# Kernel optimization log

Measured on AMD Instinct MI355X. Metric: run time of the kernel, lower is better.

## Reference

```python
import jax, jax.numpy as jnp
import numpy as np


def gru_cell(x, h, Wih, Whh, bih, bhh):
    # torch GRU cell, gate order r, z, n
    gi = x @ Wih.T + bih
    gh = h @ Whh.T + bhh
    ir, iz, inn = jnp.split(gi, 3, axis=-1)
    hr, hz, hn = jnp.split(gh, 3, axis=-1)
    r = jax.nn.sigmoid(ir + hr)
    z = jax.nn.sigmoid(iz + hz)
    n = jnp.tanh(inn + r * hn)
    return (1.0 - z) * n + z * h


def setup_inputs() -> dict:
    key = jax.random.key(0)
    ks = jax.random.split(key, 24)
    S, T, B, E, H, V = 64, 64, 32, 512, 1024, 32000
    sc_e = 1.0 / np.sqrt(E)
    sc_h = 1.0 / np.sqrt(H)

    def rn(i, shape, sc):
        return jax.random.normal(ks[i], shape, jnp.float32) * sc

    return {
        "src": jax.random.randint(ks[0], (S, B), 0, V),
        "trg": jax.random.randint(ks[1], (T, B), 0, V),
        "emb": rn(2, (V, E), 0.02),
        # encoder forward-direction GRU
        "Wih_f": rn(3, (3 * H, E), sc_e), "Whh_f": rn(4, (3 * H, H), sc_h),
        "bih_f": rn(5, (3 * H,), sc_h), "bhh_f": rn(6, (3 * H,), sc_h),
        # encoder backward-direction GRU
        "Wih_b": rn(7, (3 * H, E), sc_e), "Whh_b": rn(8, (3 * H, H), sc_h),
        "bih_b": rn(9, (3 * H,), sc_h), "bhh_b": rn(10, (3 * H,), sc_h),
        # attention: Linear(2H -> H) and scoring vector v
        "Wa": rn(11, (H, 2 * H), sc_h), "ba": rn(12, (H,), sc_h),
        "v": rn(13, (H,), sc_h),
        # decoder GRU: input is [embedded(E); context(H)]
        "Wih_d": rn(14, (3 * H, E + H), sc_h), "Whh_d": rn(15, (3 * H, H), sc_h),
        "bih_d": rn(16, (3 * H,), sc_h), "bhh_d": rn(17, (3 * H,), sc_h),
        # output head Linear(2H -> V)
        "Wout": rn(18, (V, 2 * H), sc_h), "bout": rn(19, (V,), sc_h),
    }


def reference(src, trg, emb, Wih_f, Whh_f, bih_f, bhh_f, Wih_b, Whh_b, bih_b, bhh_b,
              Wa, ba, v, Wih_d, Whh_d, bih_d, bhh_d, Wout, bout):
    S, B = src.shape
    H = Whh_f.shape[1]

    # ---- encoder: bidirectional GRU, fwd+bwd output halves summed ----
    src_emb = emb[src]  # [S, B, E]
    h0 = jnp.zeros((B, H), src_emb.dtype)

    def step_f(h, x):
        h2 = gru_cell(x, h, Wih_f, Whh_f, bih_f, bhh_f)
        return h2, h2

    def step_b(h, x):
        h2 = gru_cell(x, h, Wih_b, Whh_b, bih_b, bhh_b)
        return h2, h2

    h_fwd, out_f = jax.lax.scan(step_f, h0, src_emb)
    _, out_b_rev = jax.lax.scan(step_b, h0, src_emb[::-1])
    enc_out = out_f + out_b_rev[::-1]          # [S, B, H]
    enc_bt = enc_out.transpose(1, 0, 2)        # [B, S, H]

    # ---- decoder with teacher forcing (ratio fixed to 1.0) ----
    dec_tokens = jnp.concatenate([src[-1:], trg[:-1]], axis=0)  # [T, B]
    dec_emb = emb[dec_tokens]                                   # [T, B, E]

    def dec_step(h, e_t):
        # Bahdanau attention: relu(Linear([h; enc])) scored by v
        hrep = jnp.broadcast_to(h[:, None, :], enc_bt.shape)    # [B, S, H]
        energy = jax.nn.relu(jnp.concatenate([hrep, enc_bt], -1) @ Wa.T + ba)
        scores = energy @ v                                     # [B, S]
        a = jax.nn.softmax(scores, axis=1)
        ctx = jnp.einsum('bs,bsh->bh', a, enc_bt)               # [B, H]
        rnn_in = jnp.concatenate([e_t, ctx], axis=-1)           # [B, E+H]
        h_new = gru_cell(rnn_in, h, Wih_d, Whh_d, bih_d, bhh_d)
        logits = jnp.concatenate([h_new, ctx], -1) @ Wout.T + bout  # [B, V]
        return h_new, logits

    _, outputs = jax.lax.scan(dec_step, h_fwd, dec_emb)  # [T, B, V]
    return outputs
```

## Files before the change

kernel.cpp:

```cpp
#include <hip/hip_runtime.h>
#include <hip/hip_bf16.h>

#define S_ 64
#define T_ 64
#define B_ 32
#define E_ 512
#define H_ 1024
#define V_ 32000
#define H3 3072
#define H2 2048
#define EH 1536

typedef unsigned short u16;
typedef unsigned int u32;
typedef unsigned long long u64;
typedef __attribute__((ext_vector_type(8))) short bf16x8;
typedef __attribute__((ext_vector_type(4))) float f32x4;

#define MFMA3(ACC, AH_, AL_, BH_, BL_)                                              \
    ACC = __builtin_amdgcn_mfma_f32_16x16x32_bf16(AL_, BH_, ACC, 0, 0, 0);          \
    ACC = __builtin_amdgcn_mfma_f32_16x16x32_bf16(AH_, BL_, ACC, 0, 0, 0);          \
    ACC = __builtin_amdgcn_mfma_f32_16x16x32_bf16(AH_, BH_, ACC, 0, 0, 0);

__device__ __forceinline__ void splitf(float x, u16& h, u16& l) {
    u32 xb = __float_as_uint(x);
    u32 hb = (xb + 0x7FFFu + ((xb >> 16) & 1u)) & 0xFFFF0000u;
    h = (u16)(hb >> 16);
    float lf = x - __uint_as_float(hb);
    u32 lb = __float_as_uint(lf);
    l = (u16)((lb + 0x7FFFu + ((lb >> 16) & 1u)) >> 16);
}

__device__ __forceinline__ float bf2f(u16 v) { return __uint_as_float(((u32)v) << 16); }

__device__ __forceinline__ void load_lds16(const void* g, void* l) {
    __builtin_amdgcn_global_load_lds((const __attribute__((address_space(1))) u32*)g,
                                     (__attribute__((address_space(3))) u32*)l, 16, 0, 0);
}

__device__ __forceinline__ bf16x8 ld_sys16(const u16* p) {
    union { bf16x8 v; u64 q[2]; } u;
    const u64* q = (const u64*)p;
    u.q[0] = __hip_atomic_load(q,     __ATOMIC_RELAXED, __HIP_MEMORY_SCOPE_SYSTEM);
    u.q[1] = __hip_atomic_load(q + 1, __ATOMIC_RELAXED, __HIP_MEMORY_SCOPE_SYSTEM);
    return u.v;
}
__device__ __forceinline__ float ld_sysf(const float* p) {
    return __hip_atomic_load(p, __ATOMIC_RELAXED, __HIP_MEMORY_SCOPE_SYSTEM);
}
__device__ __forceinline__ void st_sysf(float* p, float v) {
    __hip_atomic_store(p, v, __ATOMIC_RELAXED, __HIP_MEMORY_SCOPE_SYSTEM);
}
__device__ __forceinline__ void st_sysu16(u16* p, u16 v) {
    __hip_atomic_store(p, v, __ATOMIC_RELAXED, __HIP_MEMORY_SCOPE_SYSTEM);
}

__device__ __forceinline__ void gbar(int* cnt, int* flag, int nblk, int blk, int& gen) {
    __syncthreads();
    if (threadIdx.x == 0) {
        gen += 1;
        asm volatile("s_waitcnt vmcnt(0)" ::: "memory");
        __hip_atomic_fetch_add(&cnt[(blk & 7) << 5], 1, __ATOMIC_RELAXED,
                               __HIP_MEMORY_SCOPE_SYSTEM);
        if (blk == 0) {
            const int target = nblk * gen;
            for (;;) {
                int sum = 0;
#pragma unroll
                for (int j = 0; j < 8; ++j)
                    sum += __hip_atomic_load(&cnt[j << 5], __ATOMIC_RELAXED,
                                             __HIP_MEMORY_SCOPE_SYSTEM);
                if (sum >= target) break;
                __builtin_amdgcn_s_sleep(2);
            }
#pragma unroll
            for (int j = 0; j < 8; ++j)
                __hip_atomic_store(&flag[j << 5], gen, __ATOMIC_RELAXED,
                                   __HIP_MEMORY_SCOPE_SYSTEM);
        } else {
            while (__hip_atomic_load(&flag[(blk & 7) << 5], __ATOMIC_RELAXED,
                                     __HIP_MEMORY_SCOPE_SYSTEM) < gen)
                __builtin_amdgcn_s_sleep(2);
        }
    }
    __syncthreads();
}

__global__ void k_embed_src_split(const int* __restrict__ src, const float* __restrict__ emb,
                                  u16* __restrict__ hi, u16* __restrict__ lo) {
    int row = blockIdx.x;
    int tok = src[row];
    int c = threadIdx.x * 4;
    float4 v = *reinterpret_cast<const float4*>(emb + (size_t)tok * E_ + c);
    ushort4 h, l;
    splitf(v.x, h.x, l.x); splitf(v.y, h.y, l.y);
    splitf(v.z, h.z, l.z); splitf(v.w, h.w, l.w);
    *reinterpret_cast<ushort4*>(hi + (size_t)row * E_ + c) = h;
    *reinterpret_cast<ushort4*>(lo + (size_t)row * E_ + c) = l;
}

__global__ void k_embed_dec_split(const int* __restrict__ src, const int* __restrict__ trg,
                                  const float* __restrict__ emb,
                                  u16* __restrict__ hi, u16* __restrict__ lo) {
    int row = blockIdx.x;
    int t = row >> 5, b = row & 31;
    int tok = (t == 0) ? src[(S_ - 1) * B_ + b] : trg[(t - 1) * B_ + b];
    int c = threadIdx.x * 4;
    float4 v = *reinterpret_cast<const float4*>(emb + (size_t)tok * E_ + c);
    ushort4 h, l;
    splitf(v.x, h.x, l.x); splitf(v.y, h.y, l.y);
    splitf(v.z, h.z, l.z); splitf(v.w, h.w, l.w);
    *reinterpret_cast<ushort4*>(hi + (size_t)row * E_ + c) = h;
    *reinterpret_cast<ushort4*>(lo + (size_t)row * E_ + c) = l;
}

__global__ __launch_bounds__(256) void k_split(const float* __restrict__ in, int ld, int cols4,
                                               u16* __restrict__ hi, u16* __restrict__ lo) {
    int c4 = blockIdx.x * 256 + threadIdx.x;
    if (c4 >= cols4) return;
    size_t r = blockIdx.y;
    float4 v = *reinterpret_cast<const float4*>(in + r * ld + (size_t)c4 * 4);
    ushort4 h, l;
    splitf(v.x, h.x, l.x); splitf(v.y, h.y, l.y);
    splitf(v.z, h.z, l.z); splitf(v.w, h.w, l.w);
    size_t o = (r * cols4 + c4) * 4;
    *reinterpret_cast<ushort4*>(hi + o) = h;
    *reinterpret_cast<ushort4*>(lo + o) = l;
}

__global__ __launch_bounds__(256) void k_split_sum_enc(
    const float* __restrict__ ef, const float* __restrict__ eb, float* __restrict__ es,
    u16* __restrict__ hi, u16* __restrict__ lo) {
    size_t r = blockIdx.y;
    int c4 = threadIdx.x * 4;
    float4 va = *reinterpret_cast<const float4*>(ef + r * H_ + c4);
    float4 vb = *reinterpret_cast<const float4*>(eb + r * H_ + c4);
    float4 v; v.x = va.x + vb.x; v.y = va.y + vb.y; v.z = va.z + vb.z; v.w = va.w + vb.w;
    *reinterpret_cast<float4*>(es + r * H_ + c4) = v;
    ushort4 h, l;
    splitf(v.x, h.x, l.x); splitf(v.y, h.y, l.y);
    splitf(v.z, h.z, l.z); splitf(v.w, h.w, l.w);
    *reinterpret_cast<ushort4*>(hi + r * H_ + c4) = h;
    *reinterpret_cast<ushort4*>(lo + r * H_ + c4) = l;
}

__global__ void k_wsplit_perm(const float* __restrict__ src, int ld, int coff,
                              u16* __restrict__ hi, u16* __restrict__ lo) {
    int r = blockIdx.x;
    int i = r / 3, g = r - i * 3;
    const float* p = src + (size_t)(g * H_ + i) * ld + coff;
    int c = threadIdx.x * 4;
    float4 v = *reinterpret_cast<const float4*>(p + c);
    ushort4 h, l;
    splitf(v.x, h.x, l.x); splitf(v.y, h.y, l.y);
    splitf(v.z, h.z, l.z); splitf(v.w, h.w, l.w);
    *reinterpret_cast<ushort4*>(hi + (size_t)r * H_ + c) = h;
    *reinterpret_cast<ushort4*>(lo + (size_t)r * H_ + c) = l;
}

__global__ __launch_bounds__(256, 2) void k_gemm_mfma3(
    const u16* __restrict__ Ah, const u16* __restrict__ Al,
    const u16* __restrict__ Bh, const u16* __restrict__ Bl,
    const float* __restrict__ bias, float* __restrict__ C,
    int ldc, int K)
{
    __shared__ u16 ls[4][128 * 32];
    const int tid = threadIdx.x;
    const int lane = tid & 63, w = tid >> 6;
    const int wr = w >> 1, wc = w & 1;
    const size_t m0 = (size_t)blockIdx.x * 128, n0 = (size_t)blockIdx.y * 128;

    const int c0 = (w * 2) * 64 + lane;
    const int r0 = c0 >> 2, kc0 = (c0 & 3) << 3;
    const size_t rstep = (size_t)16 * K;
    const u16* gAh = Ah + (m0 + r0) * K + kc0;
    const u16* gAl = Al + (m0 + r0) * K + kc0;
    const u16* gBh = Bh + (n0 + r0) * K + kc0;
    const u16* gBl = Bl + (n0 + r0) * K + kc0;
    const int lo0 = c0 * 8;

    const int frow = lane & 15, fk = (lane >> 4) << 3;
    const int offA = (wr * 64 + frow) * 32 + fk;
    const int offB = (wc * 64 + frow) * 32 + fk;

    f32x4 acc[4][4] = {};

    for (int k0 = 0; k0 < K; k0 += 32) {
        load_lds16(gAh + k0, &ls[0][lo0]);
        load_lds16(gAh + rstep + k0, &ls[0][lo0 + 512]);
        load_lds16(gAl + k0, &ls[1][lo0]);
        load_lds16(gAl + rstep + k0, &ls[1][lo0 + 512]);
        load_lds16(gBh + k0, &ls[2][lo0]);
        load_lds16(gBh + rstep + k0, &ls[2][lo0 + 512]);
        load_lds16(gBl + k0, &ls[3][lo0]);
        load_lds16(gBl + rstep + k0, &ls[3][lo0 + 512]);
        __syncthreads();

        bf16x8 fAh[4], fAl[4], fBh[4], fBl[4];
#pragma unroll
        for (int m = 0; m < 4; ++m) {
            fAh[m] = *reinterpret_cast<const bf16x8*>(&ls[0][offA + m * 512]);
            fAl[m] = *reinterpret_cast<const bf16x8*>(&ls[1][offA + m * 512]);
        }
#pragma unroll
        for (int n = 0; n < 4; ++n) {
            fBh[n] = *reinterpret_cast<const bf16x8*>(&ls[2][offB + n * 512]);
            fBl[n] = *reinterpret_cast<const bf16x8*>(&ls[3][offB + n * 512]);
        }
#pragma unroll
        for (int m = 0; m < 4; ++m)
#pragma unroll
            for (int n = 0; n < 4; ++n) {
                MFMA3(acc[m][n], fAh[m], fAl[m], fBh[n], fBl[n]);
            }
        __syncthreads();
    }

    const int crow0 = wr * 64 + ((lane >> 4) << 2);
    const int ccol0 = wc * 64 + (lane & 15);
#pragma unroll
    for (int n = 0; n < 4; ++n) {
        const size_t col = n0 + ccol0 + n * 16;
        const float bv = bias ? bias[col] : 0.f;
#pragma unroll
        for (int m = 0; m < 4; ++m)
#pragma unroll
            for (int r = 0; r < 4; ++r)
                C[(m0 + crow0 + m * 16 + r) * (size_t)ldc + col] = acc[m][n][r] + bv;
    }
}

__global__ __launch_bounds__(256, 2) void k_gemm_n2f(
    const u16* __restrict__ Ah, const u16* __restrict__ Al,
    const float* __restrict__ Bf,
    const float* __restrict__ bias, float* __restrict__ C,
    int ldc, int K)
{
    __shared__ u16 lsA[2][128 * 32];
    __shared__ u16 lsBh[256 * 32];
    __shared__ u16 lsBl[256 * 32];
    const int tid = threadIdx.x;
    const int lane = tid & 63, w = tid >> 6;
    const int wr = w >> 1, wc = w & 1;
    const size_t m0 = (size_t)blockIdx.x * 128, n0 = (size_t)blockIdx.y * 256;

    const int frow = lane & 15, fk = (lane >> 4) << 3;
    const int offA = (wr * 64 + frow) * 32 + fk;
    const int offB = (wc * 128 + frow) * 32 + fk;

    f32x4 acc[4][8] = {};

    for (int k0 = 0; k0 < K; k0 += 32) {
#pragma unroll
        for (int q = 0; q < 4; ++q) {
            const int chunk = (w + q * 4) * 64 + lane;
            const int local = chunk & 511;
            const u16* A = (chunk < 512) ? Ah : Al;
            load_lds16(A + (m0 + (local >> 2)) * K + k0 + ((local & 3) << 3),
                       &lsA[chunk >> 9][local * 8]);
        }
#pragma unroll
        for (int q = 0; q < 4; ++q) {
            const int c = tid + q * 256;
            const int row = c >> 2, k8 = (c & 3) << 3;
            const float* src = Bf + (size_t)(n0 + row) * K + k0 + k8;
            float4 v0 = *reinterpret_cast<const float4*>(src);
            float4 v1 = *reinterpret_cast<const float4*>(src + 4);
            union { ushort4 s[2]; bf16x8 v; } hh, ll;
            splitf(v0.x, hh.s[0].x, ll.s[0].x); splitf(v0.y, hh.s[0].y, ll.s[0].y);
            splitf(v0.z, hh.s[0].z, ll.s[0].z); splitf(v0.w, hh.s[0].w, ll.s[0].w);
            splitf(v1.x, hh.s[1].x, ll.s[1].x); splitf(v1.y, hh.s[1].y, ll.s[1].y);
            splitf(v1.z, hh.s[1].z, ll.s[1].z); splitf(v1.w, hh.s[1].w, ll.s[1].w);
            *reinterpret_cast<bf16x8*>(&lsBh[row * 32 + k8]) = hh.v;
            *reinterpret_cast<bf16x8*>(&lsBl[row * 32 + k8]) = ll.v;
        }
        __syncthreads();

        bf16x8 fAh[4], fAl[4];
#pragma unroll
        for (int m = 0; m < 4; ++m) {
            fAh[m] = *reinterpret_cast<const bf16x8*>(&lsA[0][offA + m * 512]);
            fAl[m] = *reinterpret_cast<const bf16x8*>(&lsA[1][offA + m * 512]);
        }
#pragma unroll
        for (int n = 0; n < 8; ++n) {
            bf16x8 fBh = *reinterpret_cast<const bf16x8*>(&lsBh[offB + n * 512]);
            bf16x8 fBl = *reinterpret_cast<const bf16x8*>(&lsBl[offB + n * 512]);
#pragma unroll
            for (int m = 0; m < 4; ++m) {
                MFMA3(acc[m][n], fAh[m], fAl[m], fBh, fBl);
            }
        }
        __syncthreads();
    }

    const int crow0 = wr * 64 + ((lane >> 4) << 2);
    const int ccol0 = wc * 128 + (lane & 15);
#pragma unroll
    for (int n = 0; n < 8; ++n) {
        const size_t col = n0 + ccol0 + n * 16;
        const float bv = bias ? bias[col] : 0.f;
#pragma unroll
        for (int m = 0; m < 4; ++m)
#pragma unroll
            for (int r = 0; r < 4; ++r)
                C[(m0 + crow0 + m * 16 + r) * (size_t)ldc + col] = acc[m][n][r] + bv;
    }
}

__global__ __launch_bounds__(256) void k_enc_persist(
    const u16* __restrict__ whhf_h, const u16* __restrict__ whhf_l,
    const u16* __restrict__ whhb_h, const u16* __restrict__ whhb_l,
    const float* __restrict__ gi_f, const float* __restrict__ gi_b,
    const float* __restrict__ bhh_f, const float* __restrict__ bhh_b,
    u16* __restrict__ hfH0, u16* __restrict__ hfL0,
    u16* __restrict__ hfH1, u16* __restrict__ hfL1,
    u16* __restrict__ hbH0, u16* __restrict__ hbL0,
    u16* __restrict__ hbH1, u16* __restrict__ hbL1,
    float* __restrict__ enc_f, float* __restrict__ enc_b,
    int* __restrict__ cnt, int* __restrict__ flag)
{
    __shared__ __align__(16) char smem[145792];
    u16* lAh  = (u16*)smem;
    u16* lAl  = (u16*)(smem + 65536);
    float* ex0 = (float*)(smem + 131072);
    float* ex1 = (float*)(smem + 137408);
    float* hloc = (float*)(smem + 143744);

    const int blk = blockIdx.x, tid = threadIdx.x;
    const int lane = tid & 63, w = tid >> 6;
    const int dir = blk >> 6, c = blk & 63;
    const int i0 = c * 16;
    const u16* WH = (dir ? whhb_h : whhf_h) + (size_t)c * 48 * 1024;
    const u16* WL = (dir ? whhb_l : whhf_l) + (size_t)c * 48 * 1024;
    const float* gi = dir ? gi_b : gi_f;
    const float* bhh = dir ? bhh_b : bhh_f;
    float* encd = dir ? enc_b : enc_f;
    int gen = 0;

    for (int q = tid; q < 512; q += 256) hloc[q] = 0.f;

    const int frow = lane & 15, fk8 = (lane >> 4) << 3;
    const int cb = lane & 15, rb0 = (lane >> 4) << 2;

    for (int t = 0; t < 64; ++t) {
        const int a = t & 1;
        const u16* rH = dir ? (a ? hbH1 : hbH0) : (a ? hfH1 : hfH0);
        const u16* rL = dir ? (a ? hbL1 : hbL0) : (a ? hfL1 : hfL0);
        u16* oH = dir ? (a ? hbH0 : hbH1) : (a ? hfH0 : hfH1);
        u16* oL = dir ? (a ? hbL0 : hbL1) : (a ? hfL0 : hfL1);
        const int s = dir ? 63 - t : t;

#pragma unroll
        for (int ch0 = 0; ch0 < 4096; ch0 += 256) {
            int ch = ch0 + tid;
            int r = ch >> 7, kc = (ch & 127) << 3;
            int sw = kc ^ ((r & 7) << 3);
            *(bf16x8*)&lAh[r * 1024 + sw] = ld_sys16(&rH[r * 1024 + kc]);
            *(bf16x8*)&lAl[r * 1024 + sw] = ld_sys16(&rL[r * 1024 + kc]);
        }
        __syncthreads();

#pragma unroll
        for (int jj = 0; jj < 3; ++jj) {
            const int j = w * 3 + jj;
            const int m = j & 1;
            const int n = (j >> 1) % 3;
            const int kh = j / 6;
            const int arow = m * 16 + frow;
            const int asw = (arow & 7) << 3;
            const u16* gBh = WH + (size_t)(n * 16 + frow) * 1024;
            const u16* gBl = WL + (size_t)(n * 16 + frow) * 1024;
            f32x4 acc = {};
            const int ke = kh * 512 + 512;
#pragma unroll 4
            for (int k0 = kh * 512; k0 < ke; k0 += 32) {
                int kc = k0 + fk8;
                bf16x8 aH = *(const bf16x8*)&lAh[arow * 1024 + (kc ^ asw)];
                bf16x8 aL = *(const bf16x8*)&lAl[arow * 1024 + (kc ^ asw)];
                bf16x8 bH = *(const bf16x8*)&gBh[kc];
                bf16x8 bL = *(const bf16x8*)&gBl[kc];
                MFMA3(acc, aH, aL, bH, bL);
            }
            float* exd = kh ? ex1 : ex0;
            const int pc = n * 16 + cb;
#pragma unroll
            for (int r = 0; r < 4; ++r)
                exd[pc * 33 + m * 16 + rb0 + r] = acc[r];
        }
        __syncthreads();

        {
            const int il = tid & 15, bb = tid >> 4;
            const int i = i0 + il;
#pragma unroll
            for (int q = 0; q < 2; ++q) {
                int b = bb + q * 16;
                float ghr = ex0[(3 * il + 0) * 33 + b] + ex1[(3 * il + 0) * 33 + b] + bhh[i];
                float ghz = ex0[(3 * il + 1) * 33 + b] + ex1[(3 * il + 1) * 33 + b] + bhh[H_ + i];
                float ghn = ex0[(3 * il + 2) * 33 + b] + ex1[(3 * il + 2) * 33 + b] + bhh[2 * H_ + i];
                size_t gio = (size_t)(s * B_ + b) * H3 + i;
                float gir = gi[gio], giz = gi[gio + H_], gin = gi[gio + 2 * H_];
                float rr = 1.f / (1.f + expf(-(gir + ghr)));
                float zz = 1.f / (1.f + expf(-(giz + ghz)));
                float nn = tanhf(gin + rr * ghn);
                float hold = hloc[b * 16 + il];
                float hnew = (1.f - zz) * nn + zz * hold;
                hloc[b * 16 + il] = hnew;
                u16 hh, hl; splitf(hnew, hh, hl);
                st_sysu16(&oH[b * 1024 + i], hh);
                st_sysu16(&oL[b * 1024 + i], hl);
                encd[((size_t)b * 64 + s) * H_ + i] = hnew;
            }
        }
        gbar(cnt, flag, 128, blk, gen);
    }
}

__global__ __launch_bounds__(256) void k_dec_persist(
    const u16* __restrict__ wah, const u16* __restrict__ wal,
    const u16* __restrict__ wgh, const u16* __restrict__ wgl,
    const u16* __restrict__ wdh, const u16* __restrict__ wdl,
    const float* __restrict__ gi_e, const float* __restrict__ bhh_d,
    const float* __restrict__ ep, const float* __restrict__ vvec,
    const float* __restrict__ enc,
    u16* __restrict__ hH, u16* __restrict__ hL,
    float* __restrict__ hwa, float* __restrict__ scores,
    u16* __restrict__ ctxH, u16* __restrict__ ctxL,
    float* __restrict__ states, int* __restrict__ cnt, int* __restrict__ flag)
{
    __shared__ __align__(16) char smem[140288];
    u16* lWH  = (u16*)smem;
    u16* lWL  = (u16*)(smem + 32768);
    u16* lDH  = (u16*)(smem + 65536);
    float* lenc = (float*)(smem + 98304);
    float* ex1a = (float*)(smem + 131072);
    float* ex1b = (float*)(smem + 133120);
    float* ex2a = (float*)(smem + 135168);
    float* ex2b = (float*)(smem + 137216);
    float* aw   = (float*)(smem + 139264);
    float* hloc = (float*)(smem + 139520);

    const int bid = blockIdx.x, tid = threadIdx.x;
    const int lane = tid & 63, w = tid >> 6;
    const int frow = lane & 15, fk8 = (lane >> 4) << 3;
    const int b3 = bid >> 3, sl = bid & 7;
    int gen = 0;

    for (int ch = tid; ch < 2048; ch += 256) {
        int r = ch >> 7, kc = (ch & 127) << 3;
        int sw = kc ^ ((r & 7) << 3);
        const u16 *sH, *sL;
        if (r < 4) { sH = wah + ((size_t)bid * 4 + r) * 1024;
                     sL = wal + ((size_t)bid * 4 + r) * 1024; }
        else       { sH = wgh + ((size_t)bid * 12 + r - 4) * 1024;
                     sL = wgl + ((size_t)bid * 12 + r - 4) * 1024; }
        *(bf16x8*)&lWH[r * 1024 + sw] = *(const bf16x8*)&sH[kc];
        *(bf16x8*)&lWL[r * 1024 + sw] = *(const bf16x8*)&sL[kc];
    }
    for (int ch = tid; ch < 2048; ch += 256) {
        int r = ch >> 7, kc = (ch & 127) << 3;
        int sw = kc ^ ((r & 7) << 3);
        int rowg = (r < 12) ? bid * 12 + r : bid * 12;
        *(bf16x8*)&lDH[r * 1024 + sw] = *(const bf16x8*)&wdh[(size_t)rowg * 1024 + kc];
    }
    for (int ch = tid; ch < 2048; ch += 256) {
        int s = ch >> 5, c4 = (ch & 31) << 2;
        *(float4*)&lenc[s * 128 + c4] =
            *(const float4*)&enc[((size_t)b3 * 64 + s) * 1024 + sl * 128 + c4];
    }
    if (tid < 128) {
        int b = tid >> 2, u = bid * 4 + (tid & 3);
        hloc[tid] = bf2f(hH[b * 1024 + u]) + bf2f(hL[b * 1024 + u]);
    }
    float vreg[16];
#pragma unroll
    for (int i = 0; i < 16; ++i) vreg[i] = vvec[lane + i * 64];
    __syncthreads();

    const int mt = w & 1, kh = w >> 1;
    const int bsw = (frow & 7) << 3;
    const int rowg = (frow < 12) ? bid * 12 + frow : bid * 12;
    const u16* gDl = wdl + (size_t)rowg * 1024;
    const int exw = (mt * 16 + ((lane >> 4) << 2)) * 16 + frow;
    const float* epr0 = ep + ((size_t)b3 * 64 + sl * 8 + w * 2) * 1024;
    const float* epr1 = epr0 + 1024;

    for (int t = 0; t < 64; ++t) {
        float pe0[16], pe1[16];
#pragma unroll
        for (int i = 0; i < 16; ++i) pe0[i] = epr0[lane + i * 64];
#pragma unroll
        for (int i = 0; i < 16; ++i) pe1[i] = epr1[lane + i * 64];
        {
            float* exA = kh ? ex1b : ex1a;
            f32x4 acc = {};
            const int ar0 = (mt * 16 + frow) * 1024;
            const int ke = kh * 512 + 512;
#pragma unroll 4
            for (int k0 = kh * 512; k0 < ke; k0 += 32) {
                int kc = k0 + fk8;
                bf16x8 aH = ld_sys16(&hH[ar0 + kc]);
                bf16x8 aL = ld_sys16(&hL[ar0 + kc]);
                bf16x8 bH = *(const bf16x8*)&lWH[frow * 1024 + (kc ^ bsw)];
                bf16x8 bL = *(const bf16x8*)&lWL[frow * 1024 + (kc ^ bsw)];
                MFMA3(acc, aH, aL, bH, bL);
            }
#pragma unroll
            for (int r = 0; r < 4; ++r) exA[exw + r * 16] = acc[r];
        }
        __syncthreads();
        if (tid < 128) {
            int b = tid >> 2, col = tid & 3;
            st_sysf(&hwa[b * 1024 + bid * 4 + col],
                    ex1a[b * 16 + col] + ex1b[b * 16 + col]);
        }
        gbar(cnt, flag, 256, bid, gen);

        {
            float hreg[16];
#pragma unroll
            for (int i = 0; i < 16; ++i)
                hreg[i] = ld_sysf(&hwa[b3 * 1024 + lane + i * 64]);
            float a2 = 0.f, a3 = 0.f;
#pragma unroll
            for (int i = 0; i < 16; ++i) {
                a2 += fmaxf(hreg[i] + pe0[i], 0.f) * vreg[i];
                a3 += fmaxf(hreg[i] + pe1[i], 0.f) * vreg[i];
            }
            for (int off = 32; off; off >>= 1) a2 += __shfl_down(a2, off);
            for (int off = 32; off; off >>= 1) a3 += __shfl_down(a3, off);
            if (lane == 0) {
                st_sysf(&scores[b3 * 64 + sl * 8 + w * 2], a2);
                st_sysf(&scores[b3 * 64 + sl * 8 + w * 2 + 1], a3);
            }
        }
        gbar(cnt, flag, 256, bid, gen);

        if (tid < 64) {
            float sc = ld_sysf(&scores[b3 * 64 + tid]);
            float m = sc;
            for (int off = 32; off; off >>= 1) m = fmaxf(m, __shfl_xor(m, off));
            float e = expf(sc - m);
            float sum = e;
            for (int off = 32; off; off >>= 1) sum += __shfl_xor(sum, off);
            aw[tid] = e / sum;
        }
        __syncthreads();
        if (tid < 128) {
            int c = tid;
            float x = 0.f;
#pragma unroll 8
            for (int s = 0; s < 64; ++s) x += aw[s] * lenc[s * 128 + c];
            states[((size_t)t * 32 + b3) * 2048 + 1024 + sl * 128 + c] = x;
            u16 hh, hl; splitf(x, hh, hl);
            st_sysu16(&ctxH[b3 * 1024 + sl * 128 + c], hh);
            st_sysu16(&ctxL[b3 * 1024 + sl * 128 + c], hl);
        }
        gbar(cnt, flag, 256, bid, gen);

        {
            float* exD = kh ? ex2b : ex2a;
            f32x4 acc = {};
            const int ar0 = (mt * 16 + frow) * 1024;
            const int ke = kh * 512 + 512;
#pragma unroll 4
            for (int k0 = kh * 512; k0 < ke; k0 += 32) {
                int kc = k0 + fk8;
                bf16x8 aH = ld_sys16(&ctxH[ar0 + kc]);
                bf16x8 aL = ld_sys16(&ctxL[ar0 + kc]);
                bf16x8 bH = *(const bf16x8*)&lDH[frow * 1024 + (kc ^ bsw)];
                bf16x8 bL = *(const bf16x8*)&gDl[kc];
                MFMA3(acc, aH, aL, bH, bL);
            }
#pragma unroll
            for (int r = 0; r < 4; ++r) exD[exw + r * 16] = acc[r];
        }
        __syncthreads();
        if (tid < 128) {
            int b = tid >> 2, ui = tid & 3;
            int u = bid * 4 + ui;
            float gicr = ex2a[b * 16 + 3 * ui + 0] + ex2b[b * 16 + 3 * ui + 0];
            float gicz = ex2a[b * 16 + 3 * ui + 1] + ex2b[b * 16 + 3 * ui + 1];
            float gicn = ex2a[b * 16 + 3 * ui + 2] + ex2b[b * 16 + 3 * ui + 2];
            float ghr = ex1a[b * 16 + 4 + 3 * ui + 0] + ex1b[b * 16 + 4 + 3 * ui + 0] + bhh_d[u];
            float ghz = ex1a[b * 16 + 4 + 3 * ui + 1] + ex1b[b * 16 + 4 + 3 * ui + 1] + bhh_d[H_ + u];
            float ghn = ex1a[b * 16 + 4 + 3 * ui + 2] + ex1b[b * 16 + 4 + 3 * ui + 2] + bhh_d[2 * H_ + u];
            size_t ge = ((size_t)t * 32 + b) * 3072;
            float gir = gi_e[ge + u] + gicr;
            float giz = gi_e[ge + 1024 + u] + gicz;
            float gin = gi_e[ge + 2048 + u] + gicn;
            float rr = 1.f / (1.f + expf(-(gir + ghr)));
            float zz = 1.f / (1.f + expf(-(giz + ghz)));
            float nn = tanhf(gin + rr * ghn);
            float hold = hloc[tid];
            float hnew = (1.f - zz) * nn + zz * hold;
            hloc[tid] = hnew;
            u16 hh, hl; splitf(hnew, hh, hl);
            st_sysu16(&hH[b * 1024 + u], hh);
            st_sysu16(&hL[b * 1024 + u], hl);
            states[((size_t)t * 32 + b) * 2048 + u] = hnew;
        }
        gbar(cnt, flag, 256, bid, gen);
    }
}

extern "C" void kernel_launch(void* const* d_in, const int* in_sizes, int n_in,
                              void* d_out, int out_size, void* d_ws, size_t ws_size,
                              hipStream_t stream) {
    const int*   src   = (const int*)d_in[0];
    const int*   trg   = (const int*)d_in[1];
    const float* emb   = (const float*)d_in[2];
    const float* Wih_f = (const float*)d_in[3];
    const float* Whh_f = (const float*)d_in[4];
    const float* bih_f = (const float*)d_in[5];
    const float* bhh_f = (const float*)d_in[6];
    const float* Wih_b = (const float*)d_in[7];
    const float* Whh_b = (const float*)d_in[8];
    const float* bih_b = (const float*)d_in[9];
    const float* bhh_b = (const float*)d_in[10];
    const float* Wa    = (const float*)d_in[11];
    const float* ba    = (const float*)d_in[12];
    const float* vv    = (const float*)d_in[13];
    const float* Wih_d = (const float*)d_in[14];
    const float* Whh_d = (const float*)d_in[15];
    const float* bih_d = (const float*)d_in[16];
    const float* bhh_d = (const float*)d_in[17];
    const float* Wout  = (const float*)d_in[18];
    const float* bout  = (const float*)d_in[19];
    float* out = (float*)d_out;
    (void)in_sizes; (void)n_in; (void)out_size; (void)ws_size;

    float* w = (float*)d_ws;
    size_t o = 0;
    auto alloc = [&](size_t n) { float* p = w + o; o += n; return p; };
    float* gi_f  = alloc((size_t)S_ * B_ * H3);
    float* gi_b  = alloc((size_t)S_ * B_ * H3);
    float* enc_f = alloc((size_t)B_ * S_ * H_);
    float* enc_b = alloc((size_t)B_ * S_ * H_);
    float* enc   = alloc((size_t)B_ * S_ * H_);
    float* ep    = alloc((size_t)B_ * S_ * H_);
    float* hwa   = alloc((size_t)B_ * H_);
    float* scores = alloc(B_ * S_);
    float* barf  = alloc(1024);
    int* cntE  = (int*)barf;
    int* flagE = cntE + 256;
    int* cntD  = cntE + 512;
    int* flagD = cntE + 768;
    float* gi_e   = gi_f;
    float* states = gi_b;

    u16* wu = (u16*)(w + o);
    size_t ou = 0;
    auto alloc16 = [&](size_t n) { u16* p = wu + ou; ou += n; return p; };
    u16* semb_h  = alloc16((size_t)S_ * B_ * E_);  u16* semb_l  = alloc16((size_t)S_ * B_ * E_);
    u16* demb_h  = alloc16((size_t)T_ * B_ * E_);  u16* demb_l  = alloc16((size_t)T_ * B_ * E_);
    u16* wihf_h  = alloc16((size_t)H3 * E_);       u16* wihf_l  = alloc16((size_t)H3 * E_);
    u16* wihb_h  = alloc16((size_t)H3 * E_);       u16* wihb_l  = alloc16((size_t)H3 * E_);
    u16* wihd_h  = alloc16((size_t)H3 * E_);       u16* wihd_l  = alloc16((size_t)H3 * E_);
    u16* wae_h   = alloc16((size_t)H_ * H_);       u16* wae_l   = alloc16((size_t)H_ * H_);
    u16* enc_h   = alloc16((size_t)B_ * S_ * H_);  u16* enc_l   = alloc16((size_t)B_ * S_ * H_);
    u16* st_h    = alloc16((size_t)T_ * B_ * H2);  u16* st_l    = alloc16((size_t)T_ * B_ * H2);
    u16* whhf_h  = alloc16((size_t)H3 * H_);       u16* whhf_l  = alloc16((size_t)H3 * H_);
    u16* whhb_h  = alloc16((size_t)H3 * H_);       u16* whhb_l  = alloc16((size_t)H3 * H_);
    u16* wgh     = alloc16((size_t)H3 * H_);       u16* wgl     = alloc16((size_t)H3 * H_);
    u16* wdh     = alloc16((size_t)H3 * H_);       u16* wdl     = alloc16((size_t)H3 * H_);
    u16* wah     = alloc16((size_t)H_ * H_);       u16* wal     = alloc16((size_t)H_ * H_);
    u16* hsf_h[2] = {alloc16(B_ * H_), alloc16(B_ * H_)};
    u16* hsf_l[2] = {alloc16(B_ * H_), alloc16(B_ * H_)};
    u16* hsb_h[2] = {alloc16(B_ * H_), alloc16(B_ * H_)};
    u16* hsb_l[2] = {alloc16(B_ * H_), alloc16(B_ * H_)};
    u16* ctx_h   = alloc16(B_ * H_);               u16* ctx_l   = alloc16(B_ * H_);

    hipMemsetAsync(barf, 0, 1024 * sizeof(float), stream);
    hipMemsetAsync(hsf_h[0], 0, B_ * H_ * sizeof(u16), stream);
    hipMemsetAsync(hsf_l[0], 0, B_ * H_ * sizeof(u16), stream);
    hipMemsetAsync(hsb_h[0], 0, B_ * H_ * sizeof(u16), stream);
    hipMemsetAsync(hsb_l[0], 0, B_ * H_ * sizeof(u16), stream);

    k_embed_src_split<<<S_ * B_, 128, 0, stream>>>(src, emb, semb_h, semb_l);
    k_embed_dec_split<<<T_ * B_, 128, 0, stream>>>(src, trg, emb, demb_h, demb_l);

    k_split<<<dim3(1, H3), 256, 0, stream>>>(Wih_f, E_, E_ / 4, wihf_h, wihf_l);
    k_split<<<dim3(1, H3), 256, 0, stream>>>(Wih_b, E_, E_ / 4, wihb_h, wihb_l);
    k_split<<<dim3(1, H3), 256, 0, stream>>>(Wih_d, EH, E_ / 4, wihd_h, wihd_l);
    k_split<<<dim3(1, H_), 256, 0, stream>>>(Wa + H_, H2, H_ / 4, wae_h, wae_l);
    k_split<<<dim3(1, H_), 256, 0, stream>>>(Wa, H2, H_ / 4, wah, wal);
    k_wsplit_perm<<<H3, 256, 0, stream>>>(Whh_f, H_, 0, whhf_h, whhf_l);
    k_wsplit_perm<<<H3, 256, 0, stream>>>(Whh_b, H_, 0, whhb_h, whhb_l);
    k_wsplit_perm<<<H3, 256, 0, stream>>>(Whh_d, H_, 0, wgh, wgl);
    k_wsplit_perm<<<H3, 256, 0, stream>>>(Wih_d, EH, E_, wdh, wdl);

    k_gemm_mfma3<<<dim3(16, 24), 256, 0, stream>>>(semb_h, semb_l, wihf_h, wihf_l,
                                                   bih_f, gi_f, H3, E_);
    k_gemm_mfma3<<<dim3(16, 24), 256, 0, stream>>>(semb_h, semb_l, wihb_h, wihb_l,
                                                   bih_b, gi_b, H3, E_);

    k_enc_persist<<<128, 256, 0, stream>>>(
        whhf_h, whhf_l, whhb_h, whhb_l, gi_f, gi_b, bhh_f, bhh_b,
        hsf_h[0], hsf_l[0], hsf_h[1], hsf_l[1],
        hsb_h[0], hsb_l[0], hsb_h[1], hsb_l[1],
        enc_f, enc_b, cntE, flagE);

    k_split_sum_enc<<<dim3(1, B_ * S_), 256, 0, stream>>>(enc_f, enc_b, enc, enc_h, enc_l);
    k_gemm_mfma3<<<dim3(16, 8), 256, 0, stream>>>(enc_h, enc_l, wae_h, wae_l,
                                                  ba, ep, H_, H_);
    k_gemm_mfma3<<<dim3(16, 24), 256, 0, stream>>>(demb_h, demb_l, wihd_h, wihd_l,
                                                   bih_d, gi_e, H3, E_);

    k_dec_persist<<<256, 256, 0, stream>>>(
        wah, wal, wgh, wgl, wdh, wdl, gi_e, bhh_d, ep, vv, enc,
        hsf_h[0], hsf_l[0], hwa, scores, ctx_h, ctx_l, states, cntD, flagD);

    k_split<<<dim3(2, T_ * B_), 256, 0, stream>>>(states, H2, H2 / 4, st_h, st_l);
    k_gemm_n2f<<<dim3(16, 125), 256, 0, stream>>>(st_h, st_l, Wout, bout, out, V_, H2);
}
```

Before: 4.069 ms.

## Narrow grid barriers to per-direction and per-batch-group scopes

The encoder's persistent kernel now synchronises the forward and backward directions with separate 64-block barriers instead of one 128-block barrier, since the two recurrences are independent. In the decoder, the two barriers around the attention score/softmax/context phase become 8-block group barriers keyed by batch group, because only blocks sharing a batch group exchange scores and context. The barrier counter area is enlarged to hold the extra counters. This is meant to cut cross-device barrier latency and straggler waiting, but it relies on the data dependencies really being confined to those groups.

```diff
diff --git a/kernel.cpp b/kernel.cpp
--- a/kernel.cpp
+++ b/kernel.cpp
@@ -82,6 +82,21 @@
                                      __HIP_MEMORY_SCOPE_SYSTEM) < gen)
                 __builtin_amdgcn_s_sleep(2);
         }
+    }
+    __syncthreads();
+}
+
+__device__ __forceinline__ void gbar_grp(int* cnt, int grp, int n, int& gen) {
+    __syncthreads();
+    if (threadIdx.x == 0) {
+        gen += 1;
+        asm volatile("s_waitcnt vmcnt(0)" ::: "memory");
+        __hip_atomic_fetch_add(&cnt[grp << 5], 1, __ATOMIC_RELAXED,
+                               __HIP_MEMORY_SCOPE_SYSTEM);
+        const int target = n * gen;
+        while (__hip_atomic_load(&cnt[grp << 5], __ATOMIC_RELAXED,
+                                 __HIP_MEMORY_SCOPE_SYSTEM) < target)
+            __builtin_amdgcn_s_sleep(1);
     }
     __syncthreads();
 }
@@ -336,6 +351,8 @@
     const float* gi = dir ? gi_b : gi_f;
     const float* bhh = dir ? bhh_b : bhh_f;
     float* encd = dir ? enc_b : enc_f;
+    int* cntd  = cnt + dir * 256;
+    int* flagd = flag + dir * 256;
     int gen = 0;
 
     for (int q = tid; q < 512; q += 256) hloc[q] = 0.f;
@@ -413,7 +430,7 @@
                 encd[((size_t)b * 64 + s) * H_ + i] = hnew;
             }
         }
-        gbar(cnt, flag, 128, blk, gen);
+        gbar(cntd, flagd, 64, c, gen);
     }
 }
 
@@ -427,7 +444,8 @@
     u16* __restrict__ hH, u16* __restrict__ hL,
     float* __restrict__ hwa, float* __restrict__ scores,
     u16* __restrict__ ctxH, u16* __restrict__ ctxL,
-    float* __restrict__ states, int* __restrict__ cnt, int* __restrict__ flag)
+    float* __restrict__ states, int* __restrict__ cnt, int* __restrict__ flag,
+    int* __restrict__ grpc)
 {
     __shared__ __align__(16) char smem[140288];
     u16* lWH  = (u16*)smem;
@@ -445,7 +463,7 @@
     const int lane = tid & 63, w = tid >> 6;
     const int frow = lane & 15, fk8 = (lane >> 4) << 3;
     const int b3 = bid >> 3, sl = bid & 7;
-    int gen = 0;
+    int gen = 0, genG = 0;
 
     for (int ch = tid; ch < 2048; ch += 256) {
         int r = ch >> 7, kc = (ch & 127) << 3;
@@ -535,7 +553,7 @@
                 st_sysf(&scores[b3 * 64 + sl * 8 + w * 2 + 1], a3);
             }
         }
-        gbar(cnt, flag, 256, bid, gen);
+        gbar_grp(grpc, b3, 8, genG);
 
         if (tid < 64) {
             float sc = ld_sysf(&scores[b3 * 64 + tid]);
@@ -557,7 +575,7 @@
             st_sysu16(&ctxH[b3 * 1024 + sl * 128 + c], hh);
             st_sysu16(&ctxL[b3 * 1024 + sl * 128 + c], hl);
         }
-        gbar(cnt, flag, 256, bid, gen);
+        gbar_grp(grpc, b3, 8, genG);
 
         {
             float* exD = kh ? ex2b : ex2a;
@@ -642,11 +660,12 @@
     float* ep    = alloc((size_t)B_ * S_ * H_);
     float* hwa   = alloc((size_t)B_ * H_);
     float* scores = alloc(B_ * S_);
-    float* barf  = alloc(1024);
+    float* barf  = alloc(4096);
     int* cntE  = (int*)barf;
-    int* flagE = cntE + 256;
-    int* cntD  = cntE + 512;
-    int* flagD = cntE + 768;
+    int* flagE = cntE + 512;
+    int* cntD  = cntE + 1024;
+    int* flagD = cntE + 1280;
+    int* grpD  = cntE + 1536;
     float* gi_e   = gi_f;
     float* states = gi_b;
 
@@ -672,7 +691,7 @@
     u16* hsb_l[2] = {alloc16(B_ * H_), alloc16(B_ * H_)};
     u16* ctx_h   = alloc16(B_ * H_);               u16* ctx_l   = alloc16(B_ * H_);
 
-    hipMemsetAsync(barf, 0, 1024 * sizeof(float), stream);
+    hipMemsetAsync(barf, 0, 4096 * sizeof(float), stream);
     hipMemsetAsync(hsf_h[0], 0, B_ * H_ * sizeof(u16), stream);
     hipMemsetAsync(hsf_l[0], 0, B_ * H_ * sizeof(u16), stream);
     hipMemsetAsync(hsb_h[0], 0, B_ * H_ * sizeof(u16), stream);
@@ -710,7 +729,7 @@
 
     k_dec_persist<<<256, 256, 0, stream>>>(
         wah, wal, wgh, wgl, wdh, wdl, gi_e, bhh_d, ep, vv, enc,
-        hsf_h[0], hsf_l[0], hwa, scores, ctx_h, ctx_l, states, cntD, flagD);
+        hsf_h[0], hsf_l[0], hwa, scores, ctx_h, ctx_l, states, cntD, flagD, grpD);
 
     k_split<<<dim3(2, T_ * B_), 256, 0, stream>>>(states, H2, H2 / 4, st_h, st_l);
     k_gemm_n2f<<<dim3(16, 125), 256, 0, stream>>>(st_h, st_l, Wout, bout, out, V_, H2);
```

Measured after the change: 3.998 ms. No clear change (-1.8%).
